# Performance work log

Measured on AMD Instinct MI355X. Metric: run time of the kernel, lower is better.

## Reference

```python
import jax, jax.numpy as jnp
import numpy as np

B, S, D = 4, 2048, 512
H = 8
DK = D // H
F = 2048  # filter_size
K = 9     # kernel_size
PAD = (K - 1) // 2
EPS = 1e-5


def layer_norm(x, gamma, beta):
    mu = jnp.mean(x, axis=-1, keepdims=True)
    var = jnp.var(x, axis=-1, keepdims=True)
    return (x - mu) * jax.lax.rsqrt(var + EPS) * gamma + beta


def conv1d(x_bcs, w_oik, b):
    # x: (B, C, S), w: (O, I, K) torch Conv1d layout, SAME padding
    y = jax.lax.conv_general_dilated(
        x_bcs, w_oik, window_strides=(1,), padding=[(PAD, PAD)],
        dimension_numbers=("NCH", "OIH", "NCH"))
    return y + b[None, :, None]


def setup_inputs() -> dict:
    key = jax.random.key(0)
    ks = jax.random.split(key, 16)
    g = lambda k, shp: (jax.random.normal(k, shp, dtype=jnp.float32) * 0.02)
    return {
        "src": jax.random.normal(ks[0], (B, S, D), dtype=jnp.float32),
        "src_mask": jnp.ones((B, 1, S), dtype=bool),
        "wq": g(ks[1], (D, D)), "bq": jnp.zeros((D,), jnp.float32),
        "wk": g(ks[2], (D, D)), "bk": jnp.zeros((D,), jnp.float32),
        "wv": g(ks[3], (D, D)), "bv": jnp.zeros((D,), jnp.float32),
        "wo": g(ks[4], (D, D)), "bo": jnp.zeros((D,), jnp.float32),
        "conv1_w": g(ks[5], (F, D, K)), "conv1_b": jnp.zeros((F,), jnp.float32),
        "conv2_w": g(ks[6], (D, F, K)), "conv2_b": jnp.zeros((D,), jnp.float32),
        "g1": jnp.ones((D,), jnp.float32), "b1": jnp.zeros((D,), jnp.float32),
        "g2": jnp.ones((D,), jnp.float32), "b2": jnp.zeros((D,), jnp.float32),
    }


def reference(src, src_mask, wq, bq, wk, bk, wv, bv, wo, bo,
              conv1_w, conv1_b, conv2_w, conv2_b, g1, b1, g2, b2):
    # ---- multi-head self attention (naive, explicit score matrix) ----
    q = (src @ wq.T + bq).reshape(B, S, H, DK).transpose(0, 2, 1, 3)  # (B,H,S,DK)
    k = (src @ wk.T + bk).reshape(B, S, H, DK).transpose(0, 2, 1, 3)
    v = (src @ wv.T + bv).reshape(B, S, H, DK).transpose(0, 2, 1, 3)
    scores = jnp.einsum("bhqd,bhkd->bhqk", q, k) / jnp.sqrt(jnp.float32(DK))
    mask4 = src_mask[:, None, :, :]  # (B,1,1,S) broadcast over heads/queries
    scores = jnp.where(mask4, scores, jnp.float32(-1e9))
    attn = jax.nn.softmax(scores, axis=-1)
    ctx = jnp.einsum("bhqk,bhkd->bhqd", attn, v)
    ctx = ctx.transpose(0, 2, 1, 3).reshape(B, S, D)
    attn_out = ctx @ wo.T + bo
    x = layer_norm(src + attn_out, g1, b1)
    # ---- conv1d FFN ----
    h = x.transpose(0, 2, 1)                       # (B, D, S)
    h = jax.nn.relu(conv1d(h, conv1_w, conv1_b))   # (B, F, S)
    h = conv1d(h, conv2_w, conv2_b)                # (B, D, S)
    ffn_out = h.transpose(0, 2, 1)
    return layer_norm(x + ffn_out, g2, b2)
```

## Files before the change

### kernel.cpp

```cpp
#include <hip/hip_runtime.h>


#define DEV __device__ __forceinline__

typedef __attribute__((ext_vector_type(8))) short bf16x8_t;
typedef __attribute__((ext_vector_type(4))) float f32x4_t;

DEV unsigned short f2bf(float f) {
  union { float f; unsigned u; } c; c.f = f;
  return (unsigned short)((c.u + 0x7fffu + ((c.u >> 16) & 1u)) >> 16);
}
DEV float bf2f(unsigned short h) {
  union { unsigned u; float f; } c; c.u = ((unsigned)h) << 16;
  return c.f;
}

DEV void stage16(const unsigned short* g, unsigned short* lds_base, int lane) {
#if __has_builtin(__builtin_amdgcn_global_load_lds)
  (void)lane;
  __builtin_amdgcn_global_load_lds(
      (const __attribute__((address_space(1))) void*)g,
      (__attribute__((address_space(3))) void*)lds_base, 16, 0, 0);
#else
  *(bf16x8_t*)(lds_base + lane * 8) = *(const bf16x8_t*)g;
#endif
}

template <int CK, int OUTMODE, int N, int K, int LDA, int LDO, int KSPLIT>
__global__ __launch_bounds__(256, 4) void gemm_bt(
    const unsigned short* __restrict__ A, const unsigned short* __restrict__ B,
    const float* __restrict__ bias, void* __restrict__ out, void* __restrict__ out2,
    long pstride) {
  __shared__ __align__(16) unsigned short As[2][128 * 32];
  __shared__ __align__(16) unsigned short Bs[2][128 * 32];
  const int tid = threadIdx.x;
  const int lane = tid & 63, wave = tid >> 6;
  const int quad = lane >> 4, l16 = lane & 15;
  const int bm = blockIdx.x << 7, bn = blockIdx.y << 7;
  const int wr = (wave >> 1) << 6, wc = (wave & 1) << 6;
  const int k0 = blockIdx.z * KSPLIT;

  f32x4_t acc[4][4];
#pragma unroll
  for (int i = 0; i < 4; i++)
#pragma unroll
    for (int j = 0; j < 4; j++) acc[i][j] = (f32x4_t){0.f, 0.f, 0.f, 0.f};

  const int srow = (wave << 4) + (lane >> 2);
  const int scol = (lane & 3) << 3;

#pragma unroll 1
  for (int kb = 0; kb < KSPLIT; kb += 64) {
    __syncthreads();
#pragma unroll
    for (int h = 0; h < 2; h++) {
      const int k = k0 + kb + (h << 5);
      int ktap, kcol;
      if (CK > 0) { ktap = k / CK; kcol = k % CK; } else { ktap = 0; kcol = k; }
#pragma unroll
      for (int i = 0; i < 2; i++) {
        const int r = (i << 6) + srow;
        const int am = bm + r;
        const int arow = (CK > 0) ? (am + ((am >> 11) << 3) + ktap) : am;
        stage16(A + (long)arow * LDA + kcol + scol, &As[h][(i << 11) + (wave << 9)], lane);
        stage16(B + (long)(bn + r) * K + k + scol, &Bs[h][(i << 11) + (wave << 9)], lane);
      }
    }
    __syncthreads();

#pragma unroll
    for (int h = 0; h < 2; h++) {
      bf16x8_t af[4], bfr[4];
#pragma unroll
      for (int t = 0; t < 4; t++)
        af[t] = *(const bf16x8_t*)&As[h][((wr + (t << 4) + l16) << 5) + (quad << 3)];
#pragma unroll
      for (int t = 0; t < 4; t++)
        bfr[t] = *(const bf16x8_t*)&Bs[h][((wc + (t << 4) + l16) << 5) + (quad << 3)];
#pragma unroll
      for (int mt = 0; mt < 4; mt++)
#pragma unroll
        for (int nt = 0; nt < 4; nt++)
          acc[mt][nt] = __builtin_amdgcn_mfma_f32_16x16x32_bf16(af[mt], bfr[nt],
                                                                acc[mt][nt], 0, 0, 0);
    }
  }

  if (OUTMODE == 4) {
    const bool isqk = (blockIdx.y < 8);
#pragma unroll
    for (int mt = 0; mt < 4; mt++)
#pragma unroll
      for (int nt = 0; nt < 4; nt++) {
        const int col = bn + wc + (nt << 4) + l16;
        const float bv = bias[col];
        const int rowb = bm + wr + (mt << 4) + (quad << 2);
        if (isqk) {
#pragma unroll
          for (int r = 0; r < 4; r++)
            ((unsigned short*)out)[(long)(rowb + r) * 1024 + col] =
                f2bf(acc[mt][nt][r] + bv);
        } else {
          ushort4 pk;
          pk.x = f2bf(acc[mt][nt][0] + bv);
          pk.y = f2bf(acc[mt][nt][1] + bv);
          pk.z = f2bf(acc[mt][nt][2] + bv);
          pk.w = f2bf(acc[mt][nt][3] + bv);
          const int vcol = col - 1024;
          const int bb = rowb >> 11, s = rowb & 2047;
          *(ushort4*)((unsigned short*)out2 + ((long)(bb * 512 + vcol) << 11) + s) = pk;
        }
      }
    return;
  }

  unsigned short* po = (unsigned short*)out;
  if (OUTMODE == 3)
    po = (blockIdx.z == 3) ? (unsigned short*)out2
                           : (unsigned short*)out + (long)blockIdx.z * pstride;
  float* fo = (float*)out;
  if (OUTMODE == 1) fo = (blockIdx.z == 0) ? (float*)out : (float*)out2;

#pragma unroll
  for (int mt = 0; mt < 4; mt++)
#pragma unroll
    for (int nt = 0; nt < 4; nt++) {
      const int col = bn + wc + (nt << 4) + l16;
      float bv = 0.f;
      if (OUTMODE == 0 || OUTMODE == 2) bv = bias[col];
      if (OUTMODE == 1) bv = (blockIdx.z == 0) ? bias[col] : 0.f;
#pragma unroll
      for (int r = 0; r < 4; r++) {
        const int row = bm + wr + (mt << 4) + (quad << 2) + r;
        float v = acc[mt][nt][r] + bv;
        if (OUTMODE == 0) {
          ((unsigned short*)out)[(long)row * LDO + col] = f2bf(v);
        } else if (OUTMODE == 1) {
          fo[(long)row * LDO + col] = v;
        } else if (OUTMODE == 2) {
          v = v > 0.f ? v : 0.f;
          const int orow = row + ((row >> 11) << 3) + 4;
          ((unsigned short*)out)[(long)orow * LDO + col] = f2bf(v);
        } else {
          po[(long)row * LDO + col] = f2bf(v);
        }
      }
    }
}

template <int CK, int OUTMODE, int KB, int LDA, int LDO, int KSPLIT>
__global__ __launch_bounds__(512, 2) void gemm8p(
    const unsigned short* __restrict__ A, const unsigned short* __restrict__ B,
    const float* __restrict__ bias, void* __restrict__ out,
    void* __restrict__ out2, long pstride) {
  __shared__ __align__(16) unsigned short lds[2][4][128 * 64];
  constexpr int NT = KSPLIT / 64;
  const int tid = threadIdx.x;
  const int lane = tid & 63, wave = tid >> 6;
  const int quad = lane >> 4, l16 = lane & 15;
  const int wm = wave >> 2, wn = wave & 3;
  const int bm = blockIdx.x << 8, bn = blockIdx.y << 8;
  const int k0 = blockIdx.z * KSPLIT;
  const int srow = lane >> 3;
  const int scol = ((lane & 7) ^ srow) << 3;
  const int pad8 = (bm >> 11) << 3;
  const int fc = (quad << 3) ^ ((l16 & 7) << 3);
  const int brow0 = (wn & 1) << 6;

  f32x4_t acc[8][4];
#pragma unroll
  for (int i = 0; i < 8; i++)
#pragma unroll
    for (int j = 0; j < 4; j++) acc[i][j] = (f32x4_t){0.f, 0.f, 0.f, 0.f};

  auto stageA = [&](int buf, int u, int h) {
    const int kk = k0 + (u << 6);
    int ktap = 0, kcb = kk;
    if (CK > 0) { ktap = kk / CK; kcb = kk % CK; }
#pragma unroll
    for (int i = 0; i < 2; i++) {
      const int rb = ((wave << 1) + i) << 3;
      const int am = bm + (h << 7) + rb + srow;
      const int arow = (CK > 0) ? (am + pad8 + ktap) : am;
      stage16(A + (long)arow * LDA + kcb + scol, &lds[buf][h][rb << 6], lane);
    }
  };
  auto stageB = [&](int buf, int u, int h) {
    const int kk = k0 + (u << 6);
#pragma unroll
    for (int i = 0; i < 2; i++) {
      const int rb = ((wave << 1) + i) << 3;
      stage16(B + (long)(bn + (h << 7) + rb + srow) * KB + kk + scol,
              &lds[buf][2 + h][rb << 6], lane);
    }
  };

  bf16x8_t af[4][2];
  bf16x8_t bfr[4][2];

  auto readAf = [&](int buf, int mt0) {
#pragma unroll
    for (int t = 0; t < 4; t++)
#pragma unroll
      for (int ks = 0; ks < 2; ks++) {
        const int row = ((mt0 + t) << 4) + l16;
        af[t][ks] = *(const bf16x8_t*)&lds[buf][wm][(row << 6) + (fc ^ (ks << 5))];
      }
  };
  auto readBf = [&](int buf) {
#pragma unroll
    for (int nt = 0; nt < 4; nt++)
#pragma unroll
      for (int ks = 0; ks < 2; ks++) {
        const int row = brow0 + (nt << 4) + l16;
        bfr[nt][ks] =
            *(const bf16x8_t*)&lds[buf][2 + (wn >> 1)][(row << 6) + (fc ^ (ks << 5))];
      }
  };

  stageA(0, 0, 0); stageA(0, 0, 1); stageB(0, 0, 0); stageB(0, 0, 1);
  if (NT > 1) {
    stageB(1, 1, 0); stageB(1, 1, 1);
    asm volatile("s_waitcnt vmcnt(4)" ::: "memory");
  } else {
    asm volatile("s_waitcnt vmcnt(0)" ::: "memory");
  }
  __builtin_amdgcn_s_barrier();
  __builtin_amdgcn_sched_barrier(0);
  readAf(0, 0);
  readBf(0);
  __builtin_amdgcn_sched_barrier(0);

#pragma unroll 1
  for (int u = 0; u < NT; ++u) {
    const int buf = u & 1;
    if (u + 1 < NT) { stageA(buf ^ 1, u + 1, 0); stageA(buf ^ 1, u + 1, 1); }
    __builtin_amdgcn_sched_barrier(0);
    __builtin_amdgcn_s_barrier();
    __builtin_amdgcn_sched_barrier(0);
    __builtin_amdgcn_s_setprio(1);
#pragma unroll
    for (int ks = 0; ks < 2; ks++)
#pragma unroll
      for (int t = 0; t < 4; t++)
#pragma unroll
        for (int nt = 0; nt < 4; nt++)
          acc[t][nt] = __builtin_amdgcn_mfma_f32_16x16x32_bf16(
              af[t][ks], bfr[nt][ks], acc[t][nt], 0, 0, 0);
    __builtin_amdgcn_s_setprio(0);
    __builtin_amdgcn_sched_barrier(0);
    readAf(buf, 4);
    __builtin_amdgcn_sched_barrier(0);
    if (u + 2 < NT) { stageB(buf, u + 2, 0); stageB(buf, u + 2, 1); }
    __builtin_amdgcn_sched_barrier(0);
    __builtin_amdgcn_s_barrier();
    __builtin_amdgcn_sched_barrier(0);
    __builtin_amdgcn_s_setprio(1);
#pragma unroll
    for (int ks = 0; ks < 2; ks++)
#pragma unroll
      for (int t = 0; t < 4; t++)
#pragma unroll
        for (int nt = 0; nt < 4; nt++)
          acc[4 + t][nt] = __builtin_amdgcn_mfma_f32_16x16x32_bf16(
              af[t][ks], bfr[nt][ks], acc[4 + t][nt], 0, 0, 0);
    __builtin_amdgcn_s_setprio(0);
    __builtin_amdgcn_sched_barrier(0);
    if (u + 1 < NT) {
      if (u + 2 < NT) asm volatile("s_waitcnt vmcnt(4)" ::: "memory");
      else            asm volatile("s_waitcnt vmcnt(0)" ::: "memory");
      readAf(buf ^ 1, 0);
      readBf(buf ^ 1);
    }
    __builtin_amdgcn_sched_barrier(0);
  }

  unsigned short* po = (unsigned short*)out;
  if (OUTMODE == 3)
    po = (blockIdx.z == 3) ? (unsigned short*)out2
                           : (unsigned short*)out + (long)blockIdx.z * pstride;
#pragma unroll
  for (int mt = 0; mt < 8; mt++)
#pragma unroll
    for (int nt = 0; nt < 4; nt++) {
      const int col = bn + (wn << 6) + (nt << 4) + l16;
      float bv = 0.f;
      if (OUTMODE == 2) bv = bias[col];
#pragma unroll
      for (int r = 0; r < 4; r++) {
        const int row = bm + (wm << 7) + (mt << 4) + (quad << 2) + r;
        float v = acc[mt][nt][r] + bv;
        if (OUTMODE == 2) {
          v = v > 0.f ? v : 0.f;
          const int orow = row + ((row >> 11) << 3) + 4;
          po[(long)orow * LDO + col] = f2bf(v);
        } else {
          po[(long)row * LDO + col] = f2bf(v);
        }
      }
    }
}

__global__ __launch_bounds__(256) void flash_attn(
    const unsigned short* __restrict__ qk16, const unsigned short* __restrict__ vT,
    unsigned short* __restrict__ ctx16) {
  __shared__ __align__(16) unsigned short Ks[64 * 64];
  __shared__ __align__(16) unsigned short Vt[64 * 64];
  __shared__ __align__(16) unsigned short Ps[4][2][16 * 80];

  const int tid = threadIdx.x;
  const int lane = tid & 63, wave = tid >> 6;
  const int quad = lane >> 4, l16 = lane & 15;
  const int qt = blockIdx.x, bh = blockIdx.y;
  const int b = bh >> 3, h = bh & 7;
  const long rowbase = (long)b << 11;
  const int hoff = h << 6;
  const int qbase = (qt << 7) + (wave << 5);

  bf16x8_t qa[2][2];
#pragma unroll
  for (int hh = 0; hh < 2; hh++) {
    const long qrow = rowbase + qbase + (hh << 4) + l16;
    qa[hh][0] = *(const bf16x8_t*)(qk16 + (qrow << 10) + hoff + (quad << 3));
    qa[hh][1] = *(const bf16x8_t*)(qk16 + (qrow << 10) + hoff + 32 + (quad << 3));
  }
  bf16x8_t ones;
#pragma unroll
  for (int i = 0; i < 8; i++) ones[i] = (short)0x3F80;

  f32x4_t o[2][4];
#pragma unroll
  for (int hh = 0; hh < 2; hh++)
#pragma unroll
    for (int i = 0; i < 4; i++) o[hh][i] = (f32x4_t){0.f, 0.f, 0.f, 0.f};
  f32x4_t l4[2] = {{0.f, 0.f, 0.f, 0.f}, {0.f, 0.f, 0.f, 0.f}};

  const int srow8 = lane >> 3;
  const int scol8 = (lane & 7) << 3;
  const unsigned short* kbase = qk16 + 512;
  const unsigned short* vbase = vT + ((long)(b * 512 + hoff) << 11);

  for (int kt = 0; kt < 2048; kt += 64) {
    __syncthreads();
#pragma unroll
    for (int j = 0; j < 2; j++) {
      const int kr = (wave << 4) + (j << 3);
      stage16(kbase + ((rowbase + kt + kr + srow8) << 10) + hoff + scol8,
              &Ks[kr << 6], lane);
      stage16(vbase + ((long)(kr + srow8) << 11) + kt + scol8, &Vt[kr << 6], lane);
    }
    __syncthreads();

    bf16x8_t kf[4][2];
#pragma unroll
    for (int t = 0; t < 4; t++) {
      kf[t][0] = *(const bf16x8_t*)&Ks[(((t << 4) + l16) << 6) + (quad << 3)];
      kf[t][1] = *(const bf16x8_t*)&Ks[(((t << 4) + l16) << 6) + 32 + (quad << 3)];
    }
#pragma unroll
    for (int hh = 0; hh < 2; hh++) {
      f32x4_t s[4];
#pragma unroll
      for (int t = 0; t < 4; t++) s[t] = (f32x4_t){0.f, 0.f, 0.f, 0.f};
#pragma unroll
      for (int t = 0; t < 4; t++) {
        s[t] = __builtin_amdgcn_mfma_f32_16x16x32_bf16(qa[hh][0], kf[t][0], s[t], 0, 0, 0);
        s[t] = __builtin_amdgcn_mfma_f32_16x16x32_bf16(qa[hh][1], kf[t][1], s[t], 0, 0, 0);
      }
#pragma unroll
      for (int r = 0; r < 4; r++)
#pragma unroll
        for (int t = 0; t < 4; t++) {
          union { float f; unsigned u; } cv;
          cv.f = __expf(s[t][r] * 0.125f);
          Ps[wave][hh][((quad << 2) + r) * 80 + (t << 4) + l16] =
              (unsigned short)(cv.u >> 16);
        }
    }
    bf16x8_t vf[4][2];
#pragma unroll
    for (int t = 0; t < 4; t++) {
      vf[t][0] = *(const bf16x8_t*)&Vt[(((t << 4) + l16) << 6) + (quad << 3)];
      vf[t][1] = *(const bf16x8_t*)&Vt[(((t << 4) + l16) << 6) + 32 + (quad << 3)];
    }
#pragma unroll
    for (int hh = 0; hh < 2; hh++) {
      const bf16x8_t pa0 = *(const bf16x8_t*)&Ps[wave][hh][l16 * 80 + (quad << 3)];
      const bf16x8_t pa1 = *(const bf16x8_t*)&Ps[wave][hh][l16 * 80 + 32 + (quad << 3)];
      l4[hh] = __builtin_amdgcn_mfma_f32_16x16x32_bf16(pa0, ones, l4[hh], 0, 0, 0);
      l4[hh] = __builtin_amdgcn_mfma_f32_16x16x32_bf16(pa1, ones, l4[hh], 0, 0, 0);
#pragma unroll
      for (int dt = 0; dt < 4; dt++) {
        o[hh][dt] = __builtin_amdgcn_mfma_f32_16x16x32_bf16(pa0, vf[dt][0], o[hh][dt], 0, 0, 0);
        o[hh][dt] = __builtin_amdgcn_mfma_f32_16x16x32_bf16(pa1, vf[dt][1], o[hh][dt], 0, 0, 0);
      }
    }
  }

#pragma unroll
  for (int hh = 0; hh < 2; hh++)
#pragma unroll
    for (int r = 0; r < 4; r++) {
      const float inv = 1.f / l4[hh][r];
      const long orow = rowbase + qbase + (hh << 4) + (quad << 2) + r;
#pragma unroll
      for (int dt = 0; dt < 4; dt++)
        ctx16[(orow << 9) + hoff + (dt << 4) + l16] = f2bf(o[hh][dt][r] * inv);
    }
}

__global__ __launch_bounds__(256) void ln_fused(
    const float* __restrict__ xa, const float* __restrict__ xb,
    const float* __restrict__ xc, const float* __restrict__ gamma,
    const float* __restrict__ beta, unsigned short* __restrict__ padout) {
  const int lane = threadIdx.x & 63, wave = threadIdx.x >> 6;
  const long row = ((long)blockIdx.x << 2) + wave;
  const long base = (row << 9) + (lane << 3);
  float s[8];
  {
    const float4 a0 = *(const float4*)(xa + base);
    const float4 a1 = *(const float4*)(xa + base + 4);
    const float4 b0 = *(const float4*)(xb + base);
    const float4 b1 = *(const float4*)(xb + base + 4);
    const float4 c0 = *(const float4*)(xc + base);
    const float4 c1 = *(const float4*)(xc + base + 4);
    s[0] = a0.x + b0.x + c0.x; s[1] = a0.y + b0.y + c0.y;
    s[2] = a0.z + b0.z + c0.z; s[3] = a0.w + b0.w + c0.w;
    s[4] = a1.x + b1.x + c1.x; s[5] = a1.y + b1.y + c1.y;
    s[6] = a1.z + b1.z + c1.z; s[7] = a1.w + b1.w + c1.w;
  }
  float sum = 0.f, sq = 0.f;
#pragma unroll
  for (int i = 0; i < 8; i++) { sum += s[i]; sq += s[i] * s[i]; }
#pragma unroll
  for (int d = 1; d < 64; d <<= 1) { sum += __shfl_xor(sum, d); sq += __shfl_xor(sq, d); }
  const float mean = sum * (1.f / 512.f);
  const float var = sq * (1.f / 512.f) - mean * mean;
  const float rstd = rsqrtf(var + 1e-5f);
  const int col = lane << 3;
  const long prow = row + ((row >> 11) << 3) + 4;
  bf16x8_t pv;
#pragma unroll
  for (int i = 0; i < 8; i++)
    pv[i] = (short)f2bf((s[i] - mean) * rstd * gamma[col + i] + beta[col + i]);
  *(bf16x8_t*)(padout + (prow << 9) + (lane << 3)) = pv;
}

__global__ __launch_bounds__(256) void ln2_red(
    const unsigned short* __restrict__ xpad, const unsigned short* __restrict__ pA,
    const unsigned short* __restrict__ pB, const float* __restrict__ bias,
    const float* __restrict__ gamma, const float* __restrict__ beta,
    float* __restrict__ out) {
  const int lane = threadIdx.x & 63, wave = threadIdx.x >> 6;
  const long row = ((long)blockIdx.x << 2) + wave;
  const long base = (row << 9) + (lane << 3);
  const int col = lane << 3;
  const long prow = row + ((row >> 11) << 3) + 4;
  const bf16x8_t xr = *(const bf16x8_t*)(xpad + (prow << 9) + (lane << 3));
  const bf16x8_t p0 = *(const bf16x8_t*)(pA + base);
  const bf16x8_t p1 = *(const bf16x8_t*)(pA + 4194304 + base);
  const bf16x8_t p2 = *(const bf16x8_t*)(pA + 8388608 + base);
  const bf16x8_t p3 = *(const bf16x8_t*)(pB + base);
  float s[8];
#pragma unroll
  for (int i = 0; i < 8; i++) {
    s[i] = bf2f((unsigned short)xr[i]) + bias[col + i] +
           bf2f((unsigned short)p0[i]) + bf2f((unsigned short)p1[i]) +
           bf2f((unsigned short)p2[i]) + bf2f((unsigned short)p3[i]);
  }
  float sum = 0.f, sq = 0.f;
#pragma unroll
  for (int i = 0; i < 8; i++) { sum += s[i]; sq += s[i] * s[i]; }
#pragma unroll
  for (int d = 1; d < 64; d <<= 1) { sum += __shfl_xor(sum, d); sq += __shfl_xor(sq, d); }
  const float mean = sum * (1.f / 512.f);
  const float var = sq * (1.f / 512.f) - mean * mean;
  const float rstd = rsqrtf(var + 1e-5f);
  float y[8];
#pragma unroll
  for (int i = 0; i < 8; i++) y[i] = (s[i] - mean) * rstd * gamma[col + i] + beta[col + i];
  float4 y0 = {y[0], y[1], y[2], y[3]}, y1 = {y[4], y[5], y[6], y[7]};
  *(float4*)(out + base) = y0;
  *(float4*)(out + base + 4) = y1;
}

__global__ void prep(const float* __restrict__ src, unsigned short* __restrict__ src16,
                     const float* __restrict__ wq, const float* __restrict__ wk,
                     const float* __restrict__ wv, const float* __restrict__ wo,
                     unsigned short* __restrict__ wqkv16, unsigned short* __restrict__ wo16,
                     const float* __restrict__ c1w, unsigned short* __restrict__ w1p,
                     const float* __restrict__ c2w, unsigned short* __restrict__ w2p,
                     unsigned short* __restrict__ xpad,
                     const float* __restrict__ bq, const float* __restrict__ bk,
                     const float* __restrict__ bv, float* __restrict__ bqkv) {
  const int bid = blockIdx.x, tid = threadIdx.x;
  if (bid < 4096) {
    const int i = bid * 256 + tid;
    const float4 v = ((const float4*)src)[i];
    ushort4 r; r.x = f2bf(v.x); r.y = f2bf(v.y); r.z = f2bf(v.z); r.w = f2bf(v.w);
    ((ushort4*)src16)[i] = r;
  } else if (bid < 5120) {
    const int w = (bid - 4096) >> 8;
    const int i = ((bid - 4096) & 255) * 256 + tid;
    const float* sp = (w == 0) ? wq : (w == 1) ? wk : (w == 2) ? wv : wo;
    unsigned short* dp = (w < 3) ? (wqkv16 + (w << 18)) : wo16;
    const float4 v = ((const float4*)sp)[i];
    ushort4 r; r.x = f2bf(v.x); r.y = f2bf(v.y); r.z = f2bf(v.z); r.w = f2bf(v.w);
    ((ushort4*)dp)[i] = r;
  } else if (bid < 9216) {
    const int idx = (bid - 5120) * 256 + tid;
    const int c = idx & 511, f = idx >> 9;
    float vals[9];
#pragma unroll
    for (int k = 0; k < 9; k++) vals[k] = c1w[(long)idx * 9 + k];
#pragma unroll
    for (int k = 0; k < 9; k++)
      w1p[(((long)f * 9 + k) << 9) + c] = f2bf(vals[k]);
  } else if (bid < 13312) {
    const int idx = (bid - 9216) * 256 + tid;
    const int c = idx & 2047, f = idx >> 11;
    float vals[9];
#pragma unroll
    for (int k = 0; k < 9; k++) vals[k] = c2w[(long)idx * 9 + k];
#pragma unroll
    for (int k = 0; k < 9; k++)
      w2p[(((long)f * 9 + k) << 11) + c] = f2bf(vals[k]);
  } else if (bid < 13376) {
    const int i = (bid - 13312) * 256 + tid;
    const int b = i >> 12, r = (i >> 9) & 7, c = i & 511;
    const int t = (r < 4) ? r : 2048 + r;
    xpad[((long)b * 2056 + t) * 512 + c] = 0;
  } else {
    const int i = (bid - 13376) * 256 + tid;
    bqkv[i] = (i < 512) ? bq[i] : (i < 1024) ? bk[i - 512] : bv[i - 1024];
  }
}

__global__ void zero_hpad(unsigned short* __restrict__ hpad) {
  const long j = (long)blockIdx.x * 256 + threadIdx.x;
  const int b = j >> 14, r = (j >> 11) & 7, c = j & 2047;
  const int t = (r < 4) ? r : 2048 + r;
  hpad[((long)b * 2056 + t) * 2048 + c] = 0;
}

extern "C" void kernel_launch(void* const* d_in, const int* in_sizes, int n_in,
                              void* d_out, int out_size, void* d_ws, size_t ws_size,
                              hipStream_t stream) {
  (void)in_sizes; (void)n_in; (void)out_size; (void)ws_size;
  const float* src = (const float*)d_in[0];
  const float* wq = (const float*)d_in[2];  const float* bq = (const float*)d_in[3];
  const float* wk = (const float*)d_in[4];  const float* bk = (const float*)d_in[5];
  const float* wv = (const float*)d_in[6];  const float* bv = (const float*)d_in[7];
  const float* wo = (const float*)d_in[8];  const float* bo = (const float*)d_in[9];
  const float* c1w = (const float*)d_in[10]; const float* c1b = (const float*)d_in[11];
  const float* c2w = (const float*)d_in[12]; const float* c2b = (const float*)d_in[13];
  const float* g1 = (const float*)d_in[14]; const float* b1 = (const float*)d_in[15];
  const float* g2 = (const float*)d_in[16]; const float* b2 = (const float*)d_in[17];
  float* out = (float*)d_out;

  char* ws = (char*)d_ws;
  unsigned short* src16  = (unsigned short*)(ws + 0);
  unsigned short* wqkv16 = (unsigned short*)(ws + 8388608);
  unsigned short* wo16   = wqkv16 + 786432;
  unsigned short* qk16   = (unsigned short*)(ws + 10485760);
  float* proj1           = (float*)(ws + 10485760);
  unsigned short* vT     = (unsigned short*)(ws + 27262976);
  unsigned short* ctx16  = (unsigned short*)(ws + 35651584);
  float* bqkv            = (float*)(ws + 35651584);
  float* attn_out        = (float*)(ws + 44040192);
  unsigned short* xpad   = (unsigned short*)(ws + 77594624);
  unsigned short* w1p    = (unsigned short*)(ws + 86016000);
  unsigned short* w2p    = (unsigned short*)(ws + 104890368);
  unsigned short* hpad   = (unsigned short*)(ws + 0);
  unsigned short* pA     = (unsigned short*)(ws + 35651584);
  unsigned short* pB     = (unsigned short*)(ws + 60817408);

  prep<<<13382, 256, 0, stream>>>(src, src16, wq, wk, wv, wo, wqkv16, wo16,
                                  c1w, w1p, c2w, w2p, xpad, bq, bk, bv, bqkv);

  gemm_bt<0, 4, 1536, 512, 512, 1024, 512><<<dim3(64, 12, 1), 256, 0, stream>>>(
      src16, wqkv16, bqkv, qk16, vT, 0);

  flash_attn<<<dim3(16, 32), 256, 0, stream>>>(qk16, vT, ctx16);

  gemm_bt<0, 1, 512, 512, 512, 512, 256><<<dim3(64, 4, 2), 256, 0, stream>>>(
      ctx16, wo16, bo, attn_out, proj1, 0);

  ln_fused<<<2048, 256, 0, stream>>>(src, attn_out, proj1, g1, b1, xpad);

  zero_hpad<<<256, 256, 0, stream>>>(hpad);

  gemm8p<512, 2, 4608, 512, 2048, 4608><<<dim3(32, 8, 1), 512, 0, stream>>>(
      xpad, w1p, c1b, hpad, nullptr, 0);

  gemm8p<2048, 3, 18432, 2048, 512, 4608><<<dim3(32, 2, 4), 512, 0, stream>>>(
      hpad, w2p, nullptr, pA, pB, 4194304);

  ln2_red<<<2048, 256, 0, stream>>>(xpad, pA, pB, c2b, g2, b2, out);
}
```

Measured before the change: 516.8 us.

## Double-buffer MFMA fragments and interleave LDS reads with MFMAs in gemm8p

Restructures the gemm8p main loop to unroll by two k-steps, using ping-pong register fragments (even/odd A and B) so LDS reads for the next half-tile are issued alongside the current MFMA block instead of after it. sched_group_barrier hints interleave ds_read instructions between MFMAs to hide LDS latency, and an explicit epilogue replaces the runtime tail conditions. This costs extra VGPRs for the duplicated fragments, which may pressure the 512-thread, 2-block launch bounds, and it requires NT to be even and at least 4.

New measurement: 531.6 us. 1.03x slower.

```diff
diff --git a/kernel.cpp b/kernel.cpp
--- a/kernel.cpp
+++ b/kernel.cpp
@@ -148,6 +148,23 @@
     }
 }
 
+#define MFMA_CL(AF, BF, MT0)                                              \
+  {                                                                       \
+    _Pragma("unroll") for (int ks_ = 0; ks_ < 2; ks_++)                   \
+    _Pragma("unroll") for (int t_ = 0; t_ < 4; t_++)                      \
+    _Pragma("unroll") for (int nt_ = 0; nt_ < 4; nt_++)                   \
+      acc[(MT0) + t_][nt_] = __builtin_amdgcn_mfma_f32_16x16x32_bf16(     \
+          AF[t_][ks_], BF[nt_][ks_], acc[(MT0) + t_][nt_], 0, 0, 0);      \
+  }
+
+#define SGB_MFMA_DS(MF, DS, REP)                                          \
+  {                                                                       \
+    _Pragma("unroll") for (int i_ = 0; i_ < (REP); i_++) {                \
+      __builtin_amdgcn_sched_group_barrier(0x008, (MF), 0);               \
+      __builtin_amdgcn_sched_group_barrier(0x100, (DS), 0);               \
+    }                                                                     \
+  }
+
 template <int CK, int OUTMODE, int KB, int LDA, int LDO, int KSPLIT>
 __global__ __launch_bounds__(512, 2) void gemm8p(
     const unsigned short* __restrict__ A, const unsigned short* __restrict__ B,
@@ -155,6 +172,7 @@
     void* __restrict__ out2, long pstride) {
   __shared__ __align__(16) unsigned short lds[2][4][128 * 64];
   constexpr int NT = KSPLIT / 64;
+  static_assert(NT >= 4 && (NT & 1) == 0, "NT must be even and >= 4");
   const int tid = threadIdx.x;
   const int lane = tid & 63, wave = tid >> 6;
   const int quad = lane >> 4, l16 = lane & 15;
@@ -195,85 +213,110 @@
     }
   };
 
-  bf16x8_t af[4][2];
-  bf16x8_t bfr[4][2];
-
-  auto readAf = [&](int buf, int mt0) {
+  bf16x8_t afE[4][2], afO[4][2], bfrE[4][2], bfrO[4][2];
+
+  auto readA = [&](bf16x8_t (&dst)[4][2], int bufi, int mt0) {
 #pragma unroll
     for (int t = 0; t < 4; t++)
 #pragma unroll
       for (int ks = 0; ks < 2; ks++) {
         const int row = ((mt0 + t) << 4) + l16;
-        af[t][ks] = *(const bf16x8_t*)&lds[buf][wm][(row << 6) + (fc ^ (ks << 5))];
+        dst[t][ks] = *(const bf16x8_t*)&lds[bufi][wm][(row << 6) + (fc ^ (ks << 5))];
       }
   };
-  auto readBf = [&](int buf) {
+  auto readB = [&](bf16x8_t (&dst)[4][2], int bufi) {
 #pragma unroll
     for (int nt = 0; nt < 4; nt++)
 #pragma unroll
       for (int ks = 0; ks < 2; ks++) {
         const int row = brow0 + (nt << 4) + l16;
-        bfr[nt][ks] =
-            *(const bf16x8_t*)&lds[buf][2 + (wn >> 1)][(row << 6) + (fc ^ (ks << 5))];
+        dst[nt][ks] =
+            *(const bf16x8_t*)&lds[bufi][2 + (wn >> 1)][(row << 6) + (fc ^ (ks << 5))];
       }
   };
 
   stageA(0, 0, 0); stageA(0, 0, 1); stageB(0, 0, 0); stageB(0, 0, 1);
-  if (NT > 1) {
-    stageB(1, 1, 0); stageB(1, 1, 1);
-    asm volatile("s_waitcnt vmcnt(4)" ::: "memory");
-  } else {
-    asm volatile("s_waitcnt vmcnt(0)" ::: "memory");
-  }
+  stageB(1, 1, 0); stageB(1, 1, 1);
+  asm volatile("s_waitcnt vmcnt(4)" ::: "memory");
   __builtin_amdgcn_s_barrier();
   __builtin_amdgcn_sched_barrier(0);
-  readAf(0, 0);
-  readBf(0);
+  readA(afE, 0, 0);
+  readB(bfrE, 0);
   __builtin_amdgcn_sched_barrier(0);
 
 #pragma unroll 1
-  for (int u = 0; u < NT; ++u) {
-    const int buf = u & 1;
-    if (u + 1 < NT) { stageA(buf ^ 1, u + 1, 0); stageA(buf ^ 1, u + 1, 1); }
+  for (int uu = 0; uu < NT - 2; uu += 2) {
+    stageA(1, uu + 1, 0); stageA(1, uu + 1, 1);
     __builtin_amdgcn_sched_barrier(0);
     __builtin_amdgcn_s_barrier();
-    __builtin_amdgcn_sched_barrier(0);
     __builtin_amdgcn_s_setprio(1);
-#pragma unroll
-    for (int ks = 0; ks < 2; ks++)
-#pragma unroll
-      for (int t = 0; t < 4; t++)
-#pragma unroll
-        for (int nt = 0; nt < 4; nt++)
-          acc[t][nt] = __builtin_amdgcn_mfma_f32_16x16x32_bf16(
-              af[t][ks], bfr[nt][ks], acc[t][nt], 0, 0, 0);
+    readA(afO, 0, 4);
+    MFMA_CL(afE, bfrE, 0);
+    SGB_MFMA_DS(4, 1, 8);
     __builtin_amdgcn_s_setprio(0);
     __builtin_amdgcn_sched_barrier(0);
-    readAf(buf, 4);
-    __builtin_amdgcn_sched_barrier(0);
-    if (u + 2 < NT) { stageB(buf, u + 2, 0); stageB(buf, u + 2, 1); }
-    __builtin_amdgcn_sched_barrier(0);
+    stageB(0, uu + 2, 0); stageB(0, uu + 2, 1);
+    __builtin_amdgcn_sched_barrier(0);
+    asm volatile("s_waitcnt vmcnt(4)" ::: "memory");
     __builtin_amdgcn_s_barrier();
-    __builtin_amdgcn_sched_barrier(0);
     __builtin_amdgcn_s_setprio(1);
-#pragma unroll
-    for (int ks = 0; ks < 2; ks++)
-#pragma unroll
-      for (int t = 0; t < 4; t++)
-#pragma unroll
-        for (int nt = 0; nt < 4; nt++)
-          acc[4 + t][nt] = __builtin_amdgcn_mfma_f32_16x16x32_bf16(
-              af[t][ks], bfr[nt][ks], acc[4 + t][nt], 0, 0, 0);
+    readA(afE, 1, 0);
+    readB(bfrO, 1);
+    MFMA_CL(afO, bfrE, 4);
+    SGB_MFMA_DS(2, 1, 16);
     __builtin_amdgcn_s_setprio(0);
     __builtin_amdgcn_sched_barrier(0);
-    if (u + 1 < NT) {
-      if (u + 2 < NT) asm volatile("s_waitcnt vmcnt(4)" ::: "memory");
-      else            asm volatile("s_waitcnt vmcnt(0)" ::: "memory");
-      readAf(buf ^ 1, 0);
-      readBf(buf ^ 1);
-    }
-    __builtin_amdgcn_sched_barrier(0);
-  }
+    stageA(0, uu + 2, 0); stageA(0, uu + 2, 1);
+    __builtin_amdgcn_sched_barrier(0);
+    __builtin_amdgcn_s_barrier();
+    __builtin_amdgcn_s_setprio(1);
+    readA(afO, 1, 4);
+    MFMA_CL(afE, bfrO, 0);
+    SGB_MFMA_DS(4, 1, 8);
+    __builtin_amdgcn_s_setprio(0);
+    __builtin_amdgcn_sched_barrier(0);
+    stageB(1, uu + 3, 0); stageB(1, uu + 3, 1);
+    __builtin_amdgcn_sched_barrier(0);
+    asm volatile("s_waitcnt vmcnt(4)" ::: "memory");
+    __builtin_amdgcn_s_barrier();
+    __builtin_amdgcn_s_setprio(1);
+    readA(afE, 0, 0);
+    readB(bfrE, 0);
+    MFMA_CL(afO, bfrO, 4);
+    SGB_MFMA_DS(2, 1, 16);
+    __builtin_amdgcn_s_setprio(0);
+    __builtin_amdgcn_sched_barrier(0);
+  }
+
+  stageA(1, NT - 1, 0); stageA(1, NT - 1, 1);
+  __builtin_amdgcn_sched_barrier(0);
+  __builtin_amdgcn_s_barrier();
+  __builtin_amdgcn_s_setprio(1);
+  readA(afO, 0, 4);
+  MFMA_CL(afE, bfrE, 0);
+  SGB_MFMA_DS(4, 1, 8);
+  __builtin_amdgcn_s_setprio(0);
+  __builtin_amdgcn_sched_barrier(0);
+  asm volatile("s_waitcnt vmcnt(0)" ::: "memory");
+  __builtin_amdgcn_s_barrier();
+  __builtin_amdgcn_s_setprio(1);
+  readA(afE, 1, 0);
+  readB(bfrO, 1);
+  MFMA_CL(afO, bfrE, 4);
+  SGB_MFMA_DS(2, 1, 16);
+  __builtin_amdgcn_s_setprio(0);
+  __builtin_amdgcn_sched_barrier(0);
+  __builtin_amdgcn_s_barrier();
+  __builtin_amdgcn_s_setprio(1);
+  readA(afO, 1, 4);
+  MFMA_CL(afE, bfrO, 0);
+  SGB_MFMA_DS(4, 1, 8);
+  __builtin_amdgcn_s_setprio(0);
+  __builtin_amdgcn_sched_barrier(0);
+  __builtin_amdgcn_s_barrier();
+  __builtin_amdgcn_s_setprio(1);
+  MFMA_CL(afO, bfrO, 4);
+  __builtin_amdgcn_s_setprio(0);
 
   unsigned short* po = (unsigned short*)out;
   if (OUTMODE == 3)
```
